# Kernel optimization log

Hardware: AMD Instinct MI355X
Metric: run time of the kernel (lower is better)

The kernel has to match this reference:

```python
import jax, jax.numpy as jnp
import numpy as np

NUM_HEADS = 8
GRAPH_DIM = 64
K_RATIO = 0.1
SIM_THRESH = 0.6


def _gat_layer(h_in, mask, W, a_src, a_dst, b):
    # PyG GATConv (heads=1, eval mode): lin (no bias), alpha = LeakyReLU(a_src.h_j + a_dst.h_i),
    # softmax over source nodes j per target i (edges given by dense mask, self loops included), + bias.
    h = h_in @ W                                   # [N, F]
    asrc = h @ a_src                               # [N] source term
    adst = h @ a_dst                               # [N] target term
    logits = jax.nn.leaky_relu(adst[:, None] + asrc[None, :], 0.2)  # [target i, source j]
    logits = jnp.where(mask.T, logits, -1e30)      # mask[j,i]: edge src j -> dst i (symmetric here)
    alpha = jax.nn.softmax(logits, axis=-1)
    return alpha @ h + b


def _forward(x, w_qkv, w_proj, b_proj, gat0_W, gat0_asrc, gat0_adst, gat0_b,
             gat1_W, gat1_asrc, gat1_adst, gat1_b, w_g2a, b_g2a):
    B, C, H, W = x.shape
    HW = H * W
    nh = NUM_HEADS
    hd = C // nh
    scale = hd ** -0.5
    x_seq = x.reshape(B, C, HW).transpose(0, 2, 1)                 # [B, HW, C]

    # ---- build_spatial_graph ----
    importance = jnp.var(x_seq, axis=-1, ddof=1)                   # torch.var default unbiased
    N = int(HW * K_RATIO)                                          # 102 nodes
    _, top_idx = jax.lax.top_k(importance, N)                      # [B, N]
    feats = jnp.take_along_axis(x_seq, top_idx[..., None], axis=1) # [B, N, C]
    fn = feats / jnp.clip(jnp.linalg.norm(feats, axis=-1, keepdims=True), 1e-12)
    sim = fn @ fn.transpose(0, 2, 1)                               # [B, N, N]
    adj = sim > SIM_THRESH
    adj = adj | jnp.eye(N, dtype=bool)                             # GATConv add_self_loops

    # ---- per-batch GAT stack + graph_to_attn ----
    def per_graph(f, m):
        g = jax.nn.relu(_gat_layer(f, m, gat0_W, gat0_asrc, gat0_adst, gat0_b))
        g = jax.nn.relu(_gat_layer(g, m, gat1_W, gat1_asrc, gat1_adst, gat1_b))
        return jax.nn.sigmoid(g @ w_g2a.T + b_g2a)                 # [N, nh]
    gw = jax.vmap(per_graph)(feats, adj)                           # [B, N, nh]

    # ---- dense multi-head attention ----
    qkv = (x_seq @ w_qkv.T).reshape(B, HW, 3, nh, hd).transpose(2, 0, 3, 1, 4)
    q, k, v = qkv[0], qkv[1], qkv[2]                               # [B, nh, HW, hd]
    scores = jnp.einsum('bhqd,bhkd->bhqk', q, k) * scale           # [B, nh, HW, HW]

    # ---- graph modulation scatter (replaces the nested python loops) ----
    vals = jnp.where(adj[..., None], gw[:, :, None, :] * gw[:, None, :, :], 0.0)  # [B, N, N, nh]
    gm = jnp.zeros_like(scores)
    bidx = jnp.arange(B)[:, None, None]
    gm = gm.at[bidx, :, top_idx[:, :, None], top_idx[:, None, :]].set(vals)
    scores = scores + gm

    attn = jax.nn.softmax(scores, axis=-1)                         # dropout is identity in eval
    out = jnp.einsum('bhqk,bhkd->bhqd', attn, v).transpose(0, 2, 1, 3).reshape(B, HW, C)
    out = out @ w_proj.T + b_proj
    return out.transpose(0, 2, 1).reshape(B, C, H, W)


def setup_inputs() -> dict:
    key = jax.random.key(0)
    ks = jax.random.split(key, 16)
    dim, gd, nh = 256, GRAPH_DIM, NUM_HEADS
    B, H, W = 8, 32, 32
    s = 0.02
    return {
        'x': jax.random.normal(ks[0], (B, dim, H, W), dtype=jnp.float32),
        'w_qkv': s * jax.random.normal(ks[1], (3 * dim, dim), dtype=jnp.float32),
        'w_proj': s * jax.random.normal(ks[2], (dim, dim), dtype=jnp.float32),
        'b_proj': jnp.zeros((dim,), dtype=jnp.float32),
        'gat0_W': s * jax.random.normal(ks[3], (dim, gd), dtype=jnp.float32),
        'gat0_asrc': s * jax.random.normal(ks[4], (gd,), dtype=jnp.float32),
        'gat0_adst': s * jax.random.normal(ks[5], (gd,), dtype=jnp.float32),
        'gat0_b': jnp.zeros((gd,), dtype=jnp.float32),
        'gat1_W': s * jax.random.normal(ks[6], (gd, gd), dtype=jnp.float32),
        'gat1_asrc': s * jax.random.normal(ks[7], (gd,), dtype=jnp.float32),
        'gat1_adst': s * jax.random.normal(ks[8], (gd,), dtype=jnp.float32),
        'gat1_b': jnp.zeros((gd,), dtype=jnp.float32),
        'w_g2a': s * jax.random.normal(ks[9], (nh, gd), dtype=jnp.float32),
        'b_g2a': jnp.zeros((nh,), dtype=jnp.float32),
    }


def reference(x, w_qkv, w_proj, b_proj, gat0_W, gat0_asrc, gat0_adst, gat0_b,
              gat1_W, gat1_asrc, gat1_adst, gat1_b, w_g2a, b_g2a):
    return _forward(x, w_qkv, w_proj, b_proj, gat0_W, gat0_asrc, gat0_adst, gat0_b,
                    gat1_W, gat1_asrc, gat1_adst, gat1_b, w_g2a, b_g2a)
```

## Files before the change

### kernel.cpp

```cpp
#include <hip/hip_runtime.h>
#include <math.h>

#define NB 8
#define CDIM 256
#define HWD 1024
#define NH 8
#define HD 32
#define NN 102
#define GD 64

typedef __attribute__((ext_vector_type(8))) short bf16x8;
typedef __attribute__((ext_vector_type(4))) float f32x4;

__device__ inline short f2bf(float f) {
  union { float f; unsigned u; } v; v.f = f;
  unsigned r = v.u + 0x7fffu + ((v.u >> 16) & 1u);
  return (short)(r >> 16);
}
__device__ inline float bf2f(short s) {
  union { unsigned u; float f; } v;
  v.u = ((unsigned)(unsigned short)s) << 16;
  return v.f;
}

__global__ __launch_bounds__(256) void transpose_k(const float* __restrict__ in,
                                                   float* __restrict__ out, int R, int C) {
  __shared__ float tile[32][33];
  int c0 = blockIdx.x * 32, r0 = blockIdx.y * 32;
  for (int i = threadIdx.y; i < 32; i += 8) {
    int r = r0 + i, c = c0 + threadIdx.x;
    if (r < R && c < C) tile[i][threadIdx.x] = in[r * C + c];
  }
  __syncthreads();
  for (int i = threadIdx.y; i < 32; i += 8) {
    int c = c0 + i, r = r0 + threadIdx.x;
    if (r < R && c < C) out[c * R + r] = tile[threadIdx.x][i];
  }
}

__global__ __launch_bounds__(256) void prep_k(const float* __restrict__ g0W,
                                              const float* __restrict__ g1W,
                                              short* __restrict__ w0bT,
                                              short* __restrict__ w1bT) {
  int t = blockIdx.x * 256 + threadIdx.x;
  if (t < 16384) {
    int c = t >> 6, f = t & 63;
    w0bT[f * 256 + c] = f2bf(g0W[t]);
  } else if (t < 20480) {
    int u2 = t - 16384;
    int c = u2 >> 6, f = u2 & 63;
    w1bT[f * 64 + c] = f2bf(g1W[u2]);
  }
}

__global__ __launch_bounds__(256) void importance_k(const float* __restrict__ x,
                                                    float* __restrict__ imp) {
  __shared__ float red[8][33];
  int bp = blockIdx.x;
  int b = bp >> 5, p0 = (bp & 31) << 5;
  int t = threadIdx.x;
  int pl = t & 31, cg = t >> 5;
  const float* xp = x + (size_t)b * CDIM * HWD + p0 + pl;
  float s = 0.f;
  for (int cc = 0; cc < 32; ++cc) s += xp[(size_t)(cg * 32 + cc) * HWD];
  red[cg][pl] = s;
  __syncthreads();
  float tot = 0.f;
  for (int g = 0; g < 8; ++g) tot += red[g][pl];
  float mean = tot * (1.f / CDIM);
  __syncthreads();
  float v = 0.f;
  for (int cc = 0; cc < 32; ++cc) {
    float d = xp[(size_t)(cg * 32 + cc) * HWD] - mean;
    v += d * d;
  }
  red[cg][pl] = v;
  __syncthreads();
  if (t < 32) {
    float vv = 0.f;
    for (int g = 0; g < 8; ++g) vv += red[g][t];
    imp[b * 1024 + p0 + t] = vv * (1.f / (CDIM - 1));
  }
}

union GraphLDS {
  struct { float sv[1024]; int si[1024]; } tk;
  struct {
    short h0T[64 * 136];
    short alphaB[102 * 136];
    short gB[102 * 72];
  } m;
};

__global__ __launch_bounds__(1024) void graph_k(
    const float* __restrict__ x, const float* __restrict__ imp,
    const short* __restrict__ w0bT, const short* __restrict__ w1bT,
    const float* __restrict__ g0as, const float* __restrict__ g0ad,
    const float* __restrict__ g0b,
    const float* __restrict__ g1as, const float* __restrict__ g1ad,
    const float* __restrict__ g1b,
    const float* __restrict__ wg2a, const float* __restrict__ bg2a,
    int* __restrict__ nodeof, short* __restrict__ fnG,
    unsigned char* __restrict__ adjG, float* __restrict__ gwb) {
  __shared__ GraphLDS u;
  __shared__ ushort adjPack[NN][8];
  __shared__ float normL[NN];
  __shared__ float asrcL[NN], adstL[NN];
  __shared__ int topiL[NN];
  int b = blockIdx.x, t = threadIdx.x;
  int wv = t >> 6, lane = t & 63, quad = lane >> 4, l16 = lane & 15;

  u.tk.sv[t] = imp[b * 1024 + t];
  u.tk.si[t] = t;
  nodeof[b * 1024 + t] = -1;
  __syncthreads();
  for (int k = 2; k <= 1024; k <<= 1) {
    for (int j = k >> 1; j > 0; j >>= 1) {
      int ixj = t ^ j;
      if (ixj > t) {
        bool up = ((t & k) == 0);
        float a = u.tk.sv[t], c = u.tk.sv[ixj];
        if ((a > c) == up) {
          u.tk.sv[t] = c; u.tk.sv[ixj] = a;
          int ti = u.tk.si[t]; u.tk.si[t] = u.tk.si[ixj]; u.tk.si[ixj] = ti;
        }
      }
      __syncthreads();
    }
  }
  if (t >= 1024 - NN) {
    int n = 1023 - t;
    int idx = u.tk.si[t];
    topiL[n] = idx;
    nodeof[b * 1024 + idx] = n;
  }
  __syncthreads();

  {
    int n = t >> 3, g = t & 7;
    if (n < NN) {
      int idx = topiL[n];
      const float* xb = x + (size_t)b * CDIM * HWD + idx;
      float vbuf[32];
      float ssl = 0.f;
#pragma unroll
      for (int cc = 0; cc < 32; ++cc) {
        float v = xb[(size_t)(g * 32 + cc) * HWD];
        vbuf[cc] = v;
        ssl += v * v;
      }
      ssl += __shfl_xor(ssl, 1);
      ssl += __shfl_xor(ssl, 2);
      ssl += __shfl_xor(ssl, 4);
      float nrm = sqrtf(ssl);
      float rn = 1.f / fmaxf(nrm, 1e-12f);
      if (g == 0) normL[n] = nrm;
      short* fp = fnG + ((size_t)b * 112 + n) * 256 + g * 32;
#pragma unroll
      for (int cc = 0; cc < 32; cc += 4) {
        short4 s4 = {f2bf(vbuf[cc] * rn), f2bf(vbuf[cc + 1] * rn),
                     f2bf(vbuf[cc + 2] * rn), f2bf(vbuf[cc + 3] * rn)};
        *(short4*)(fp + cc) = s4;
      }
    }
  }
  for (int e = t; e < 64 * 34; e += 1024) {
    int f = e / 34, c = 102 + (e % 34);
    u.m.h0T[f * 136 + c] = 0;
  }
  __syncthreads();

  for (int tile = wv; tile < 49; tile += 16) {
    int I = tile / 7, J = tile % 7;
    const short* ap = fnG + ((size_t)b * 112 + I * 16 + l16) * 256 + quad * 8;
    const short* bp = fnG + ((size_t)b * 112 + J * 16 + l16) * 256 + quad * 8;
    f32x4 acc = (f32x4){0.f, 0.f, 0.f, 0.f};
#pragma unroll
    for (int kb = 0; kb < 8; ++kb)
      acc = __builtin_amdgcn_mfma_f32_16x16x32_bf16(*(const bf16x8*)(ap + kb * 32),
                                                    *(const bf16x8*)(bp + kb * 32), acc, 0, 0, 0);
#pragma unroll
    for (int r = 0; r < 4; ++r) {
      int i = I * 16 + quad * 4 + r, j = J * 16 + l16;
      bool e = (acc[r] > 0.6f) || (i == j);
      unsigned long long m = __ballot(e);
      if (l16 == 0) {
        int row = I * 16 + quad * 4 + r;
        if (row < NN) adjPack[row][J] = (ushort)((m >> (quad * 16)) & 0xFFFFull);
      }
      if (i < NN && j < NN) adjG[(size_t)b * NN * NN + i * NN + j] = e ? 1 : 0;
    }
  }
  __syncthreads();

  for (int tile = wv; tile < 28; tile += 16) {
    int mt = tile >> 2, nt = tile & 3;
    const short* ap = fnG + ((size_t)b * 112 + mt * 16 + l16) * 256 + quad * 8;
    const short* bp = w0bT + (nt * 16 + l16) * 256 + quad * 8;
    f32x4 acc = (f32x4){0.f, 0.f, 0.f, 0.f};
#pragma unroll
    for (int kb = 0; kb < 8; ++kb)
      acc = __builtin_amdgcn_mfma_f32_16x16x32_bf16(*(const bf16x8*)(ap + kb * 32),
                                                    *(const bf16x8*)(bp + kb * 32), acc, 0, 0, 0);
    int f = nt * 16 + l16;
#pragma unroll
    for (int r = 0; r < 4; ++r) {
      int node = mt * 16 + quad * 4 + r;
      if (node < NN) u.m.h0T[f * 136 + node] = f2bf(acc[r] * normL[node]);
    }
  }
  __syncthreads();

  for (int layer = 0; layer < 2; ++layer) {
    const float* avs = layer ? g1as : g0as;
    const float* avd = layer ? g1ad : g0ad;
    const float* bias = layer ? g1b : g0b;
    {
      int n = t >> 3, g = t & 7;
      if (n < NN) {
        float s1 = 0.f, s2 = 0.f;
#pragma unroll
        for (int uu = 0; uu < 8; ++uu) {
          int f = g * 8 + uu;
          float hv = bf2f(u.m.h0T[f * 136 + n]);
          s1 += hv * avs[f];
          s2 += hv * avd[f];
        }
        s1 += __shfl_xor(s1, 1); s1 += __shfl_xor(s1, 2); s1 += __shfl_xor(s1, 4);
        s2 += __shfl_xor(s2, 1); s2 += __shfl_xor(s2, 2); s2 += __shfl_xor(s2, 4);
        if (g == 0) { asrcL[n] = s1; adstL[n] = s2; }
      }
    }
    __syncthreads();
    for (int i = wv; i < NN; i += 16) {
      float zi = adstL[i];
      int j1 = 64 + lane;
      bool e0 = (adjPack[i][lane >> 4] >> (lane & 15)) & 1;
      bool e1 = (j1 < NN) && ((adjPack[i][j1 >> 4] >> (j1 & 15)) & 1);
      float p0 = 0.f, p1 = 0.f;
      if (e0) { float z = zi + asrcL[lane]; p0 = __expf(z > 0.f ? z : 0.2f * z); }
      if (e1) { float z = zi + asrcL[j1]; p1 = __expf(z > 0.f ? z : 0.2f * z); }
      float s = p0 + p1;
      s += __shfl_xor(s, 1); s += __shfl_xor(s, 2); s += __shfl_xor(s, 4);
      s += __shfl_xor(s, 8); s += __shfl_xor(s, 16); s += __shfl_xor(s, 32);
      float inv = 1.f / s;
      u.m.alphaB[i * 136 + lane] = f2bf(p0 * inv);
      u.m.alphaB[i * 136 + 64 + lane] = f2bf(p1 * inv);
    }
    __syncthreads();
    for (int tile = wv; tile < 28; tile += 16) {
      int mt = tile >> 2, nt = tile & 3;
      int ar = mt * 16 + l16; if (ar > NN - 1) ar = NN - 1;
      const short* ap = &u.m.alphaB[ar * 136 + quad * 8];
      const short* bp = &u.m.h0T[(nt * 16 + l16) * 136 + quad * 8];
      f32x4 acc = (f32x4){0.f, 0.f, 0.f, 0.f};
#pragma unroll
      for (int kb = 0; kb < 4; ++kb)
        acc = __builtin_amdgcn_mfma_f32_16x16x32_bf16(*(const bf16x8*)(ap + kb * 32),
                                                      *(const bf16x8*)(bp + kb * 32), acc, 0, 0, 0);
      int f = nt * 16 + l16;
      float bv = bias[f];
#pragma unroll
      for (int r = 0; r < 4; ++r) {
        int i = mt * 16 + quad * 4 + r;
        if (i < NN) u.m.gB[i * 72 + f] = f2bf(fmaxf(acc[r] + bv, 0.f));
      }
    }
    __syncthreads();
    if (layer == 0) {
      for (int tile = wv; tile < 28; tile += 16) {
        int mt = tile >> 2, nt = tile & 3;
        int ar = mt * 16 + l16; if (ar > NN - 1) ar = NN - 1;
        const short* ap = &u.m.gB[ar * 72 + quad * 8];
        const short* bp = w1bT + (nt * 16 + l16) * 64 + quad * 8;
        f32x4 acc = (f32x4){0.f, 0.f, 0.f, 0.f};
#pragma unroll
        for (int kb = 0; kb < 2; ++kb)
          acc = __builtin_amdgcn_mfma_f32_16x16x32_bf16(*(const bf16x8*)(ap + kb * 32),
                                                        *(const bf16x8*)(bp + kb * 32), acc, 0, 0, 0);
        int f = nt * 16 + l16;
#pragma unroll
        for (int r = 0; r < 4; ++r) {
          int node = mt * 16 + quad * 4 + r;
          if (node < NN) u.m.h0T[f * 136 + node] = f2bf(acc[r]);
        }
      }
      __syncthreads();
    }
  }
  float* wgL = (float*)&u.m.alphaB[0];
  if (t < 512) wgL[t] = wg2a[t];
  __syncthreads();
  if (t < NN * NH) {
    int n = t >> 3, h = t & 7;
    float z = bg2a[h];
#pragma unroll
    for (int c = 0; c < GD; ++c) z += bf2f(u.m.gB[n * 72 + c]) * wgL[h * 64 + c];
    gwb[((size_t)b * NN + n) * NH + h] = 1.f / (1.f + __expf(-z));
  }
}

#define FMA16(acc, av, bv)                                                            \
  acc[0][0] += av.x * bv.x; acc[0][1] += av.x * bv.y; acc[0][2] += av.x * bv.z;       \
  acc[0][3] += av.x * bv.w;                                                           \
  acc[1][0] += av.y * bv.x; acc[1][1] += av.y * bv.y; acc[1][2] += av.y * bv.z;       \
  acc[1][3] += av.y * bv.w;                                                           \
  acc[2][0] += av.z * bv.x; acc[2][1] += av.z * bv.y; acc[2][2] += av.z * bv.z;       \
  acc[2][3] += av.z * bv.w;                                                           \
  acc[3][0] += av.w * bv.x; acc[3][1] += av.w * bv.y; acc[3][2] += av.w * bv.z;       \
  acc[3][3] += av.w * bv.w;

__global__ __launch_bounds__(256) void qkv_k(const float* __restrict__ x,
                                             const float* __restrict__ wT,
                                             short* __restrict__ qhp, short* __restrict__ qlp,
                                             short* __restrict__ khp, short* __restrict__ klp,
                                             short* __restrict__ vtp) {
  __shared__ float a_s[16][68];
  __shared__ float b_s[16][68];
  __shared__ float c_s[64][68];
  int m0 = blockIdx.x * 64, n0 = blockIdx.y * 64;
  int b = m0 >> 10, p0 = m0 & 1023;
  int t = threadIdx.x, tx = t & 15, ty = t >> 4;
  float acc[4][4] = {};
  for (int k0 = 0; k0 < 256; k0 += 16) {
    int m = t & 63, kb = t >> 6;
#pragma unroll
    for (int r = 0; r < 4; ++r) {
      int kk = kb * 4 + r;
      a_s[kk][m] = x[((size_t)b * 256 + k0 + kk) * 1024 + p0 + m];
      b_s[kk][m] = wT[(k0 + kk) * 768 + n0 + m];
    }
    __syncthreads();
#pragma unroll
    for (int kk = 0; kk < 16; ++kk) {
      float4 av = *(const float4*)&a_s[kk][ty * 4];
      float4 bv = *(const float4*)&b_s[kk][tx * 4];
      FMA16(acc, av, bv)
    }
    __syncthreads();
  }
  int qi = n0 >> 8;
  if (qi < 2) {
    const float scale = (qi == 0) ? 0.17677669529663687f : 1.f;
    short* hp = (qi == 0) ? qhp : khp;
    short* lp = (qi == 0) ? qlp : klp;
    int n = n0 + tx * 4;
    int hh = (n >> 5) & 7, d = n & 31;
#pragma unroll
    for (int i = 0; i < 4; ++i) {
      int p = p0 + ty * 4 + i;
      size_t e = ((size_t)(b * 8 + hh) * 1024 + p) * 32 + d;
      float v0 = acc[i][0] * scale, v1 = acc[i][1] * scale;
      float v2 = acc[i][2] * scale, v3 = acc[i][3] * scale;
      short4 hi, lo;
      hi.x = f2bf(v0); lo.x = f2bf(v0 - bf2f(hi.x));
      hi.y = f2bf(v1); lo.y = f2bf(v1 - bf2f(hi.y));
      hi.z = f2bf(v2); lo.z = f2bf(v2 - bf2f(hi.z));
      hi.w = f2bf(v3); lo.w = f2bf(v3 - bf2f(hi.w));
      *(short4*)(hp + e) = hi;
      *(short4*)(lp + e) = lo;
    }
  } else {
#pragma unroll
    for (int i = 0; i < 4; ++i)
      *(float4*)&c_s[ty * 4 + i][tx * 4] = *(float4*)&acc[i][0];
    __syncthreads();
    int dl = t >> 2, pg = t & 3;
    int n = n0 + dl;
    int hh = (n >> 5) & 7, d = n & 31;
    size_t rowb = (size_t)(b * 8 + hh) * 32768 + (size_t)d * 1024 + p0;
#pragma unroll
    for (int r = 0; r < 4; ++r) {
      int pl = pg * 16 + r * 4;
      short4 s4;
      s4.x = f2bf(c_s[pl + 0][dl]);
      s4.y = f2bf(c_s[pl + 1][dl]);
      s4.z = f2bf(c_s[pl + 2][dl]);
      s4.w = f2bf(c_s[pl + 3][dl]);
      *(short4*)(vtp + rowb + pl) = s4;
    }
  }
}

__global__ __launch_bounds__(256, 4) void attn_k(const short* __restrict__ qh,
                                                 const short* __restrict__ ql,
                                                 const short* __restrict__ kh,
                                                 const short* __restrict__ kl,
                                                 const short* __restrict__ vt,
                                                 const int* __restrict__ nodeof,
                                                 const float* __restrict__ gw,
                                                 const unsigned char* __restrict__ adj,
                                                 float* __restrict__ ao) {
  __shared__ __align__(16) short p_s[4][16 * 72];
  __shared__ float aw_s[4][16];
  int t = threadIdx.x;
  int wid = t >> 6, lane = t & 63, quad = lane >> 4, l16 = lane & 15;
  int bh = blockIdx.y, b = bh >> 3, h = bh & 7;
  int q0 = blockIdx.x * 64 + wid * 16;
  size_t base = (size_t)bh * 32768;
  short* pw = &p_s[wid][0];
  float* aw = &aw_s[wid][0];

  size_t qoff = base + (size_t)(q0 + l16) * 32 + quad * 8;
  bf16x8 qhf = *(const bf16x8*)(qh + qoff);
  bf16x8 qlf = *(const bf16x8*)(ql + qoff);

  int irow[4]; float grq[4];
#pragma unroll
  for (int r = 0; r < 4; ++r) {
    int qr = q0 + quad * 4 + r;
    int in_ = nodeof[b * 1024 + qr];
    irow[r] = in_;
    grq[r] = (in_ >= 0) ? gw[((size_t)b * NN + in_) * NH + h] : 0.f;
  }
  const unsigned char* adjB = adj + (size_t)b * NN * NN;

  f32x4 ot[2];
  ot[0] = (f32x4){0.f, 0.f, 0.f, 0.f};
  ot[1] = (f32x4){0.f, 0.f, 0.f, 0.f};
  float l_r[4] = {0.f, 0.f, 0.f, 0.f};

  for (int ch = 0; ch < 16; ++ch) {
    int c0 = ch * 64;
    bf16x8 khf[4], klf[4];
#pragma unroll
    for (int ni = 0; ni < 4; ++ni) {
      size_t off = base + (size_t)(c0 + ni * 16 + l16) * 32 + quad * 8;
      khf[ni] = *(const bf16x8*)(kh + off);
      klf[ni] = *(const bf16x8*)(kl + off);
    }
    bf16x8 vaf[2][2];
#pragma unroll
    for (int mi = 0; mi < 2; ++mi)
#pragma unroll
      for (int ks = 0; ks < 2; ++ks)
        vaf[mi][ks] = *(const bf16x8*)(vt + base + (size_t)(mi * 16 + l16) * 1024 +
                                       c0 + ks * 32 + quad * 8);
    int jn[4]; float gcn[4];
#pragma unroll
    for (int ni = 0; ni < 4; ++ni) {
      int j = nodeof[b * 1024 + c0 + ni * 16 + l16];
      jn[ni] = j;
      gcn[ni] = (j >= 0) ? gw[((size_t)b * NN + j) * NH + h] : 0.f;
    }
    f32x4 s[4];
#pragma unroll
    for (int ni = 0; ni < 4; ++ni) {
      f32x4 a = (f32x4){0.f, 0.f, 0.f, 0.f};
      a = __builtin_amdgcn_mfma_f32_16x16x32_bf16(qhf, khf[ni], a, 0, 0, 0);
      a = __builtin_amdgcn_mfma_f32_16x16x32_bf16(qhf, klf[ni], a, 0, 0, 0);
      a = __builtin_amdgcn_mfma_f32_16x16x32_bf16(qlf, khf[ni], a, 0, 0, 0);
      s[ni] = a;
    }
#pragma unroll
    for (int r = 0; r < 4; ++r) {
      int in_ = irow[r];
      if (in_ >= 0) {
        const unsigned char* ar = adjB + (size_t)in_ * NN;
        float g = grq[r];
#pragma unroll
        for (int ni = 0; ni < 4; ++ni)
          if (jn[ni] >= 0 && ar[jn[ni]]) s[ni][r] += g * gcn[ni];
      }
    }
#pragma unroll
    for (int r = 0; r < 4; ++r) {
      float e0 = __expf(s[0][r]);
      float e1 = __expf(s[1][r]);
      float e2 = __expf(s[2][r]);
      float e3 = __expf(s[3][r]);
      l_r[r] += (e0 + e1) + (e2 + e3);
      int prow = (quad * 4 + r) * 72;
      pw[prow + 0 + l16] = f2bf(e0);
      pw[prow + 16 + l16] = f2bf(e1);
      pw[prow + 32 + l16] = f2bf(e2);
      pw[prow + 48 + l16] = f2bf(e3);
    }
#pragma unroll
    for (int ks = 0; ks < 2; ++ks) {
      bf16x8 pb = *(const bf16x8*)(pw + l16 * 72 + ks * 32 + quad * 8);
      ot[0] = __builtin_amdgcn_mfma_f32_16x16x32_bf16(vaf[0][ks], pb, ot[0], 0, 0, 0);
      ot[1] = __builtin_amdgcn_mfma_f32_16x16x32_bf16(vaf[1][ks], pb, ot[1], 0, 0, 0);
    }
  }
#pragma unroll
  for (int r = 0; r < 4; ++r) {
    float ls = l_r[r];
    ls += __shfl_xor(ls, 1);
    ls += __shfl_xor(ls, 2);
    ls += __shfl_xor(ls, 4);
    ls += __shfl_xor(ls, 8);
    if (l16 == 0) aw[quad * 4 + r] = 1.f / ls;
  }
  float li = aw[l16];
  ot[0] *= li;
  ot[1] *= li;
  float* os = (float*)pw;
#pragma unroll
  for (int mi = 0; mi < 2; ++mi)
#pragma unroll
    for (int r = 0; r < 4; ++r)
      os[l16 * 36 + mi * 16 + quad * 4 + r] = ot[mi][r];
  int qr2 = lane >> 2, dg = (lane & 3) * 8;
  size_t ob = (size_t)(b * 1024 + q0 + qr2) * 256 + h * 32 + dg;
  *(float4*)&ao[ob] = *(float4*)&os[qr2 * 36 + dg];
  *(float4*)&ao[ob + 4] = *(float4*)&os[qr2 * 36 + dg + 4];
}

__global__ __launch_bounds__(256) void proj_k(const float* __restrict__ ao,
                                              const float* __restrict__ wT,
                                              const float* __restrict__ bias,
                                              float* __restrict__ out) {
  __shared__ float a_s[16][68];
  __shared__ float b_s[16][68];
  __shared__ float c_s[64][68];
  int m0 = blockIdx.x * 64, n0 = blockIdx.y * 64;
  int b = m0 >> 10, p0 = m0 & 1023;
  int t = threadIdx.x, tx = t & 15, ty = t >> 4;
  float acc[4][4] = {};
  for (int k0 = 0; k0 < 256; k0 += 16) {
    {
      int kk = t & 15, mm = t >> 4;
#pragma unroll
      for (int r = 0; r < 4; ++r) {
        int m = mm + r * 16;
        a_s[kk][m] = ao[(size_t)(m0 + m) * 256 + k0 + kk];
      }
      int mB = t & 63, kb = t >> 6;
#pragma unroll
      for (int r2 = 0; r2 < 4; ++r2) {
        int kk2 = kb * 4 + r2;
        b_s[kk2][mB] = wT[(k0 + kk2) * 256 + n0 + mB];
      }
    }
    __syncthreads();
#pragma unroll
    for (int kk = 0; kk < 16; ++kk) {
      float4 av = *(const float4*)&a_s[kk][ty * 4];
      float4 bv = *(const float4*)&b_s[kk][tx * 4];
      FMA16(acc, av, bv)
    }
    __syncthreads();
  }
#pragma unroll
  for (int i = 0; i < 4; ++i)
#pragma unroll
    for (int j = 0; j < 4; ++j) c_s[tx * 4 + j][ty * 4 + i] = acc[i][j];
  __syncthreads();
  {
    int cl = t >> 2, pg = t & 3;
    float bv = bias[n0 + cl];
#pragma unroll
    for (int r = 0; r < 4; ++r) {
      int p = pg * 16 + r * 4;
      float4 v4 = {c_s[cl][p] + bv, c_s[cl][p + 1] + bv, c_s[cl][p + 2] + bv, c_s[cl][p + 3] + bv};
      *(float4*)&out[((size_t)b * 256 + n0 + cl) * 1024 + p0 + p] = v4;
    }
  }
}

extern "C" void kernel_launch(void* const* d_in, const int* in_sizes, int n_in,
                              void* d_out, int out_size, void* d_ws, size_t ws_size,
                              hipStream_t stream) {
  const float* x      = (const float*)d_in[0];
  const float* w_qkv  = (const float*)d_in[1];
  const float* w_proj = (const float*)d_in[2];
  const float* b_proj = (const float*)d_in[3];
  const float* g0W    = (const float*)d_in[4];
  const float* g0as   = (const float*)d_in[5];
  const float* g0ad   = (const float*)d_in[6];
  const float* g0b    = (const float*)d_in[7];
  const float* g1W    = (const float*)d_in[8];
  const float* g1as   = (const float*)d_in[9];
  const float* g1ad   = (const float*)d_in[10];
  const float* g1b    = (const float*)d_in[11];
  const float* wg2a   = (const float*)d_in[12];
  const float* bg2a   = (const float*)d_in[13];
  float* out = (float*)d_out;
  float* ws = (float*)d_ws;

  size_t o = 0;
  auto alloc = [&](size_t nf) { float* p = ws + o; o += (nf + 15) & ~(size_t)15; return p; };
  float* wqkvT  = alloc(256 * 768);
  float* wprojT = alloc(256 * 256);
  float* imp    = alloc(8 * 1024);
  int*   nodeof = (int*)alloc(8 * 1024);
  short* fnG    = (short*)alloc(8 * 112 * 256 / 2);
  short* w0bT   = (short*)alloc(256 * 64 / 2);
  short* w1bT   = (short*)alloc(64 * 64 / 2);
  unsigned char* adj = (unsigned char*)alloc((8 * NN * NN + 3) / 4 + 16);
  float* gwb    = alloc(8 * NN * 8);
  short* qh     = (short*)alloc(1048576);
  short* ql     = (short*)alloc(1048576);
  short* kh     = (short*)alloc(1048576);
  short* kl     = (short*)alloc(1048576);
  short* vt     = (short*)alloc(1048576);
  float* ao     = alloc((size_t)8 * 1024 * 256);
  if (ws_size < o * sizeof(float)) return;

  transpose_k<<<dim3(8, 24), dim3(32, 8), 0, stream>>>(w_qkv, wqkvT, 768, 256);
  transpose_k<<<dim3(8, 8), dim3(32, 8), 0, stream>>>(w_proj, wprojT, 256, 256);
  prep_k<<<80, 256, 0, stream>>>(g0W, g1W, w0bT, w1bT);
  importance_k<<<256, 256, 0, stream>>>(x, imp);
  graph_k<<<8, 1024, 0, stream>>>(x, imp, w0bT, w1bT, g0as, g0ad, g0b,
                                  g1as, g1ad, g1b, wg2a, bg2a,
                                  nodeof, fnG, adj, gwb);
  qkv_k<<<dim3(128, 12), 256, 0, stream>>>(x, wqkvT, qh, ql, kh, kl, vt);
  attn_k<<<dim3(16, 64), 256, 0, stream>>>(qh, ql, kh, kl, vt, nodeof, gwb, adj, ao);
  proj_k<<<dim3(128, 4), 256, 0, stream>>>(ao, wprojT, b_proj, out);
}
```

Before: 349.1 us.

## Move QKV and output projections to split-bf16 MFMA with pre-split operands

Replaces the fp32 FMA tiled GEMMs for the QKV and output projections with MFMA 16x16x32 bf16 GEMMs. Each operand is split into hi and lo bf16 parts, and three MFMAs per tile recover near-fp32 accuracy. New pre-pass kernels split the weights and transpose-split x. The attention kernel now writes hi/lo bf16 outputs instead of fp32, and its grid axes are swapped. The cost is extra passes and workspace for the split tensors, direct global loads without LDS staging, and scattered scalar stores for Q/K.

```diff
diff --git a/kernel.cpp b/kernel.cpp
--- a/kernel.cpp
+++ b/kernel.cpp
@@ -23,18 +23,55 @@
   return v.f;
 }
 
-__global__ __launch_bounds__(256) void transpose_k(const float* __restrict__ in,
-                                                   float* __restrict__ out, int R, int C) {
-  __shared__ float tile[32][33];
-  int c0 = blockIdx.x * 32, r0 = blockIdx.y * 32;
-  for (int i = threadIdx.y; i < 32; i += 8) {
-    int r = r0 + i, c = c0 + threadIdx.x;
-    if (r < R && c < C) tile[i][threadIdx.x] = in[r * C + c];
-  }
-  __syncthreads();
-  for (int i = threadIdx.y; i < 32; i += 8) {
-    int c = c0 + i, r = r0 + threadIdx.x;
-    if (r < R && c < C) out[c * R + r] = tile[threadIdx.x][i];
+__global__ __launch_bounds__(256) void wsplit_k(const float* __restrict__ w_qkv,
+                                                const float* __restrict__ w_proj,
+                                                short* __restrict__ wqh, short* __restrict__ wql,
+                                                short* __restrict__ wph, short* __restrict__ wpl) {
+  int t = blockIdx.x * 256 + threadIdx.x;
+  if (t < 196608) {
+    float v = w_qkv[t];
+    short hi = f2bf(v);
+    wqh[t] = hi; wql[t] = f2bf(v - bf2f(hi));
+  } else {
+    int u = t - 196608;
+    float v = w_proj[u];
+    short hi = f2bf(v);
+    wph[u] = hi; wpl[u] = f2bf(v - bf2f(hi));
+  }
+}
+
+__global__ __launch_bounds__(256) void xsplit_k(const float* __restrict__ x,
+                                                short* __restrict__ xth,
+                                                short* __restrict__ xtl) {
+  __shared__ float tile[64][65];
+  int p0 = blockIdx.x * 64, c0 = blockIdx.y * 64, b = blockIdx.z;
+  int t = threadIdx.x;
+  {
+    int g = t >> 6, p = t & 63;
+#pragma unroll
+    for (int i = 0; i < 16; ++i) {
+      int cc = g * 16 + i;
+      tile[cc][p] = x[((size_t)(b * 256 + c0 + cc)) * 1024 + p0 + p];
+    }
+  }
+  __syncthreads();
+  {
+    int p = t >> 2, cs = (t & 3) * 16;
+    size_t rb = ((size_t)(b * 1024 + p0 + p)) * 256 + c0 + cs;
+#pragma unroll
+    for (int g = 0; g < 4; ++g) {
+      short4 hv, lv;
+      float f0 = tile[cs + g * 4 + 0][p];
+      float f1 = tile[cs + g * 4 + 1][p];
+      float f2 = tile[cs + g * 4 + 2][p];
+      float f3 = tile[cs + g * 4 + 3][p];
+      hv.x = f2bf(f0); lv.x = f2bf(f0 - bf2f(hv.x));
+      hv.y = f2bf(f1); lv.y = f2bf(f1 - bf2f(hv.y));
+      hv.z = f2bf(f2); lv.z = f2bf(f2 - bf2f(hv.z));
+      hv.w = f2bf(f3); lv.w = f2bf(f3 - bf2f(hv.w));
+      *(short4*)(xth + rb + g * 4) = hv;
+      *(short4*)(xtl + rb + g * 4) = lv;
+    }
   }
 }
 
@@ -300,85 +337,72 @@
   }
 }
 
-#define FMA16(acc, av, bv)                                                            \
-  acc[0][0] += av.x * bv.x; acc[0][1] += av.x * bv.y; acc[0][2] += av.x * bv.z;       \
-  acc[0][3] += av.x * bv.w;                                                           \
-  acc[1][0] += av.y * bv.x; acc[1][1] += av.y * bv.y; acc[1][2] += av.y * bv.z;       \
-  acc[1][3] += av.y * bv.w;                                                           \
-  acc[2][0] += av.z * bv.x; acc[2][1] += av.z * bv.y; acc[2][2] += av.z * bv.z;       \
-  acc[2][3] += av.z * bv.w;                                                           \
-  acc[3][0] += av.w * bv.x; acc[3][1] += av.w * bv.y; acc[3][2] += av.w * bv.z;       \
-  acc[3][3] += av.w * bv.w;
-
-__global__ __launch_bounds__(256) void qkv_k(const float* __restrict__ x,
-                                             const float* __restrict__ wT,
+__global__ __launch_bounds__(256) void qkv_k(const short* __restrict__ xth,
+                                             const short* __restrict__ xtl,
+                                             const short* __restrict__ wqh,
+                                             const short* __restrict__ wql,
                                              short* __restrict__ qhp, short* __restrict__ qlp,
                                              short* __restrict__ khp, short* __restrict__ klp,
                                              short* __restrict__ vtp) {
-  __shared__ float a_s[16][68];
-  __shared__ float b_s[16][68];
-  __shared__ float c_s[64][68];
-  int m0 = blockIdx.x * 64, n0 = blockIdx.y * 64;
-  int b = m0 >> 10, p0 = m0 & 1023;
-  int t = threadIdx.x, tx = t & 15, ty = t >> 4;
-  float acc[4][4] = {};
-  for (int k0 = 0; k0 < 256; k0 += 16) {
-    int m = t & 63, kb = t >> 6;
-#pragma unroll
-    for (int r = 0; r < 4; ++r) {
-      int kk = kb * 4 + r;
-      a_s[kk][m] = x[((size_t)b * 256 + k0 + kk) * 1024 + p0 + m];
-      b_s[kk][m] = wT[(k0 + kk) * 768 + n0 + m];
-    }
-    __syncthreads();
-#pragma unroll
-    for (int kk = 0; kk < 16; ++kk) {
-      float4 av = *(const float4*)&a_s[kk][ty * 4];
-      float4 bv = *(const float4*)&b_s[kk][tx * 4];
-      FMA16(acc, av, bv)
-    }
-    __syncthreads();
-  }
-  int qi = n0 >> 8;
+  __shared__ short vs_s[4][64 * 24];
+  int t = threadIdx.x, wid = t >> 6, lane = t & 63, quad = lane >> 4, l16 = lane & 15;
+  int m0 = blockIdx.x * 64, y = blockIdx.y;
+  int b = m0 >> 10;
+  int row = m0 + wid * 16 + l16;
+  int p_base = (m0 & 1023) + wid * 16;
+  int qi = y >> 2, n0 = (y & 3) * 64;
+  const short* wh = wqh + (size_t)(qi * 256 + n0) * 256;
+  const short* wl = wql + (size_t)(qi * 256 + n0) * 256;
+  const short* arh = xth + (size_t)row * 256 + quad * 8;
+  const short* arl = xtl + (size_t)row * 256 + quad * 8;
+  f32x4 acc[4];
+#pragma unroll
+  for (int nt = 0; nt < 4; ++nt) acc[nt] = (f32x4){0.f, 0.f, 0.f, 0.f};
+#pragma unroll
+  for (int kb = 0; kb < 8; ++kb) {
+    bf16x8 ah = *(const bf16x8*)(arh + kb * 32);
+    bf16x8 al = *(const bf16x8*)(arl + kb * 32);
+#pragma unroll
+    for (int nt = 0; nt < 4; ++nt) {
+      size_t wo = (size_t)(nt * 16 + l16) * 256 + kb * 32 + quad * 8;
+      bf16x8 bh_ = *(const bf16x8*)(wh + wo);
+      bf16x8 bl_ = *(const bf16x8*)(wl + wo);
+      acc[nt] = __builtin_amdgcn_mfma_f32_16x16x32_bf16(ah, bh_, acc[nt], 0, 0, 0);
+      acc[nt] = __builtin_amdgcn_mfma_f32_16x16x32_bf16(ah, bl_, acc[nt], 0, 0, 0);
+      acc[nt] = __builtin_amdgcn_mfma_f32_16x16x32_bf16(al, bh_, acc[nt], 0, 0, 0);
+    }
+  }
   if (qi < 2) {
     const float scale = (qi == 0) ? 0.17677669529663687f : 1.f;
     short* hp = (qi == 0) ? qhp : khp;
     short* lp = (qi == 0) ? qlp : klp;
-    int n = n0 + tx * 4;
-    int hh = (n >> 5) & 7, d = n & 31;
-#pragma unroll
-    for (int i = 0; i < 4; ++i) {
-      int p = p0 + ty * 4 + i;
-      size_t e = ((size_t)(b * 8 + hh) * 1024 + p) * 32 + d;
-      float v0 = acc[i][0] * scale, v1 = acc[i][1] * scale;
-      float v2 = acc[i][2] * scale, v3 = acc[i][3] * scale;
-      short4 hi, lo;
-      hi.x = f2bf(v0); lo.x = f2bf(v0 - bf2f(hi.x));
-      hi.y = f2bf(v1); lo.y = f2bf(v1 - bf2f(hi.y));
-      hi.z = f2bf(v2); lo.z = f2bf(v2 - bf2f(hi.z));
-      hi.w = f2bf(v3); lo.w = f2bf(v3 - bf2f(hi.w));
-      *(short4*)(hp + e) = hi;
-      *(short4*)(lp + e) = lo;
+#pragma unroll
+    for (int nt = 0; nt < 4; ++nt) {
+      int nq = n0 + nt * 16 + l16;
+      int h = nq >> 5, d = nq & 31;
+#pragma unroll
+      for (int r = 0; r < 4; ++r) {
+        int p = p_base + quad * 4 + r;
+        float v = acc[nt][r] * scale;
+        short hi = f2bf(v);
+        short lo = f2bf(v - bf2f(hi));
+        size_t e = ((size_t)(b * 8 + h) * 1024 + p) * 32 + d;
+        hp[e] = hi;
+        lp[e] = lo;
+      }
     }
   } else {
-#pragma unroll
-    for (int i = 0; i < 4; ++i)
-      *(float4*)&c_s[ty * 4 + i][tx * 4] = *(float4*)&acc[i][0];
-    __syncthreads();
-    int dl = t >> 2, pg = t & 3;
-    int n = n0 + dl;
-    int hh = (n >> 5) & 7, d = n & 31;
-    size_t rowb = (size_t)(b * 8 + hh) * 32768 + (size_t)d * 1024 + p0;
-#pragma unroll
-    for (int r = 0; r < 4; ++r) {
-      int pl = pg * 16 + r * 4;
-      short4 s4;
-      s4.x = f2bf(c_s[pl + 0][dl]);
-      s4.y = f2bf(c_s[pl + 1][dl]);
-      s4.z = f2bf(c_s[pl + 2][dl]);
-      s4.w = f2bf(c_s[pl + 3][dl]);
-      *(short4*)(vtp + rowb + pl) = s4;
-    }
+    short* vs = &vs_s[wid][0];
+#pragma unroll
+    for (int nt = 0; nt < 4; ++nt)
+#pragma unroll
+      for (int r = 0; r < 4; ++r)
+        vs[(nt * 16 + l16) * 24 + quad * 4 + r] = f2bf(acc[nt][r]);
+    int nq = n0 + lane;
+    int h = nq >> 5, d = nq & 31;
+    size_t rb = ((size_t)(b * 8 + h) * 32 + d) * 1024 + p_base;
+    *(bf16x8*)(vtp + rb) = *(const bf16x8*)(vs + lane * 24);
+    *(bf16x8*)(vtp + rb + 8) = *(const bf16x8*)(vs + lane * 24 + 8);
   }
 }
 
@@ -390,13 +414,14 @@
                                                  const int* __restrict__ nodeof,
                                                  const float* __restrict__ gw,
                                                  const unsigned char* __restrict__ adj,
-                                                 float* __restrict__ ao) {
+                                                 short* __restrict__ aoh,
+                                                 short* __restrict__ aol) {
   __shared__ __align__(16) short p_s[4][16 * 72];
   __shared__ float aw_s[4][16];
   int t = threadIdx.x;
   int wid = t >> 6, lane = t & 63, quad = lane >> 4, l16 = lane & 15;
-  int bh = blockIdx.y, b = bh >> 3, h = bh & 7;
-  int q0 = blockIdx.x * 64 + wid * 16;
+  int bh = blockIdx.x, b = bh >> 3, h = bh & 7;
+  int q0 = blockIdx.y * 64 + wid * 16;
   size_t base = (size_t)bh * 32768;
   short* pw = &p_s[wid][0];
   float* aw = &aw_s[wid][0];
@@ -502,61 +527,64 @@
     for (int r = 0; r < 4; ++r)
       os[l16 * 36 + mi * 16 + quad * 4 + r] = ot[mi][r];
   int qr2 = lane >> 2, dg = (lane & 3) * 8;
+  float f[8];
+  *(float4*)&f[0] = *(float4*)&os[qr2 * 36 + dg];
+  *(float4*)&f[4] = *(float4*)&os[qr2 * 36 + dg + 4];
+  bf16x8 hv, lv;
+#pragma unroll
+  for (int j = 0; j < 8; ++j) {
+    hv[j] = f2bf(f[j]);
+    lv[j] = f2bf(f[j] - bf2f(hv[j]));
+  }
   size_t ob = (size_t)(b * 1024 + q0 + qr2) * 256 + h * 32 + dg;
-  *(float4*)&ao[ob] = *(float4*)&os[qr2 * 36 + dg];
-  *(float4*)&ao[ob + 4] = *(float4*)&os[qr2 * 36 + dg + 4];
-}
-
-__global__ __launch_bounds__(256) void proj_k(const float* __restrict__ ao,
-                                              const float* __restrict__ wT,
+  *(bf16x8*)(aoh + ob) = hv;
+  *(bf16x8*)(aol + ob) = lv;
+}
+
+__global__ __launch_bounds__(256) void proj_k(const short* __restrict__ aoh,
+                                              const short* __restrict__ aol,
+                                              const short* __restrict__ wph,
+                                              const short* __restrict__ wpl,
                                               const float* __restrict__ bias,
                                               float* __restrict__ out) {
-  __shared__ float a_s[16][68];
-  __shared__ float b_s[16][68];
-  __shared__ float c_s[64][68];
+  __shared__ float os_s[4][64 * 20];
+  int t = threadIdx.x, wid = t >> 6, lane = t & 63, quad = lane >> 4, l16 = lane & 15;
   int m0 = blockIdx.x * 64, n0 = blockIdx.y * 64;
-  int b = m0 >> 10, p0 = m0 & 1023;
-  int t = threadIdx.x, tx = t & 15, ty = t >> 4;
-  float acc[4][4] = {};
-  for (int k0 = 0; k0 < 256; k0 += 16) {
-    {
-      int kk = t & 15, mm = t >> 4;
-#pragma unroll
-      for (int r = 0; r < 4; ++r) {
-        int m = mm + r * 16;
-        a_s[kk][m] = ao[(size_t)(m0 + m) * 256 + k0 + kk];
-      }
-      int mB = t & 63, kb = t >> 6;
-#pragma unroll
-      for (int r2 = 0; r2 < 4; ++r2) {
-        int kk2 = kb * 4 + r2;
-        b_s[kk2][mB] = wT[(k0 + kk2) * 256 + n0 + mB];
-      }
-    }
-    __syncthreads();
-#pragma unroll
-    for (int kk = 0; kk < 16; ++kk) {
-      float4 av = *(const float4*)&a_s[kk][ty * 4];
-      float4 bv = *(const float4*)&b_s[kk][tx * 4];
-      FMA16(acc, av, bv)
-    }
-    __syncthreads();
-  }
-#pragma unroll
-  for (int i = 0; i < 4; ++i)
-#pragma unroll
-    for (int j = 0; j < 4; ++j) c_s[tx * 4 + j][ty * 4 + i] = acc[i][j];
-  __syncthreads();
-  {
-    int cl = t >> 2, pg = t & 3;
-    float bv = bias[n0 + cl];
-#pragma unroll
-    for (int r = 0; r < 4; ++r) {
-      int p = pg * 16 + r * 4;
-      float4 v4 = {c_s[cl][p] + bv, c_s[cl][p + 1] + bv, c_s[cl][p + 2] + bv, c_s[cl][p + 3] + bv};
-      *(float4*)&out[((size_t)b * 256 + n0 + cl) * 1024 + p0 + p] = v4;
-    }
-  }
+  int b = m0 >> 10;
+  int row = m0 + wid * 16 + l16;
+  int p_base = (m0 & 1023) + wid * 16;
+  const short* arh = aoh + (size_t)row * 256 + quad * 8;
+  const short* arl = aol + (size_t)row * 256 + quad * 8;
+  f32x4 acc[4];
+#pragma unroll
+  for (int nt = 0; nt < 4; ++nt) acc[nt] = (f32x4){0.f, 0.f, 0.f, 0.f};
+#pragma unroll
+  for (int kb = 0; kb < 8; ++kb) {
+    bf16x8 ah = *(const bf16x8*)(arh + kb * 32);
+    bf16x8 al = *(const bf16x8*)(arl + kb * 32);
+#pragma unroll
+    for (int nt = 0; nt < 4; ++nt) {
+      size_t wo = (size_t)(n0 + nt * 16 + l16) * 256 + kb * 32 + quad * 8;
+      bf16x8 bh_ = *(const bf16x8*)(wph + wo);
+      bf16x8 bl_ = *(const bf16x8*)(wpl + wo);
+      acc[nt] = __builtin_amdgcn_mfma_f32_16x16x32_bf16(ah, bh_, acc[nt], 0, 0, 0);
+      acc[nt] = __builtin_amdgcn_mfma_f32_16x16x32_bf16(ah, bl_, acc[nt], 0, 0, 0);
+      acc[nt] = __builtin_amdgcn_mfma_f32_16x16x32_bf16(al, bh_, acc[nt], 0, 0, 0);
+    }
+  }
+  float* os = &os_s[wid][0];
+#pragma unroll
+  for (int nt = 0; nt < 4; ++nt) {
+    float bv = bias[n0 + nt * 16 + l16];
+#pragma unroll
+    for (int r = 0; r < 4; ++r)
+      os[(nt * 16 + l16) * 20 + quad * 4 + r] = acc[nt][r] + bv;
+  }
+  int c = n0 + lane;
+  float* orow = out + ((size_t)(b * 256 + c)) * 1024 + p_base;
+#pragma unroll
+  for (int g = 0; g < 4; ++g)
+    *(float4*)(orow + g * 4) = *(float4*)&os[lane * 20 + g * 4];
 }
 
 extern "C" void kernel_launch(void* const* d_in, const int* in_sizes, int n_in,
@@ -581,8 +609,6 @@
 
   size_t o = 0;
   auto alloc = [&](size_t nf) { float* p = ws + o; o += (nf + 15) & ~(size_t)15; return p; };
-  float* wqkvT  = alloc(256 * 768);
-  float* wprojT = alloc(256 * 256);
   float* imp    = alloc(8 * 1024);
   int*   nodeof = (int*)alloc(8 * 1024);
   short* fnG    = (short*)alloc(8 * 112 * 256 / 2);
@@ -590,22 +616,29 @@
   short* w1bT   = (short*)alloc(64 * 64 / 2);
   unsigned char* adj = (unsigned char*)alloc((8 * NN * NN + 3) / 4 + 16);
   float* gwb    = alloc(8 * NN * 8);
+  short* xth    = (short*)alloc(1048576);
+  short* xtl    = (short*)alloc(1048576);
+  short* wqh    = (short*)alloc(98304);
+  short* wql    = (short*)alloc(98304);
+  short* wph    = (short*)alloc(32768);
+  short* wpl    = (short*)alloc(32768);
   short* qh     = (short*)alloc(1048576);
   short* ql     = (short*)alloc(1048576);
   short* kh     = (short*)alloc(1048576);
   short* kl     = (short*)alloc(1048576);
   short* vt     = (short*)alloc(1048576);
-  float* ao     = alloc((size_t)8 * 1024 * 256);
+  short* aoh    = (short*)alloc(1048576);
+  short* aol    = (short*)alloc(1048576);
   if (ws_size < o * sizeof(float)) return;
 
-  transpose_k<<<dim3(8, 24), dim3(32, 8), 0, stream>>>(w_qkv, wqkvT, 768, 256);
-  transpose_k<<<dim3(8, 8), dim3(32, 8), 0, stream>>>(w_proj, wprojT, 256, 256);
+  importance_k<<<256, 256, 0, stream>>>(x, imp);
+  wsplit_k<<<1024, 256, 0, stream>>>(w_qkv, w_proj, wqh, wql, wph, wpl);
+  xsplit_k<<<dim3(16, 4, 8), 256, 0, stream>>>(x, xth, xtl);
   prep_k<<<80, 256, 0, stream>>>(g0W, g1W, w0bT, w1bT);
-  importance_k<<<256, 256, 0, stream>>>(x, imp);
   graph_k<<<8, 1024, 0, stream>>>(x, imp, w0bT, w1bT, g0as, g0ad, g0b,
                                   g1as, g1ad, g1b, wg2a, bg2a,
                                   nodeof, fnG, adj, gwb);
-  qkv_k<<<dim3(128, 12), 256, 0, stream>>>(x, wqkvT, qh, ql, kh, kl, vt);
-  attn_k<<<dim3(16, 64), 256, 0, stream>>>(qh, ql, kh, kl, vt, nodeof, gwb, adj, ao);
-  proj_k<<<dim3(128, 4), 256, 0, stream>>>(ao, wprojT, b_proj, out);
-}
+  qkv_k<<<dim3(128, 12), 256, 0, stream>>>(xth, xtl, wqh, wql, qh, ql, kh, kl, vt);
+  attn_k<<<dim3(64, 16), 256, 0, stream>>>(qh, ql, kh, kl, vt, nodeof, gwb, adj, aoh, aol);
+  proj_k<<<dim3(128, 4), 256, 0, stream>>>(aoh, aol, wph, wpl, b_proj, out);
+}
```

After: 356.1 us. 2.0% more time.
